# Kernel optimization log

Measured on AMD Instinct MI355X. Metric: run time of the kernel, lower is better.

The kernel has to match this reference:

```python
import jax, jax.numpy as jnp
import numpy as np

B, N, D, H = 64, 1025, 768, 128

def setup_inputs() -> dict:
    key = jax.random.key(0)
    ks = jax.random.split(key, 5)
    x = jax.random.normal(ks[0], (B, N, D), dtype=jnp.float32)
    ln_w = jnp.ones((D,), dtype=jnp.float32)
    ln_b = jnp.zeros((D,), dtype=jnp.float32)
    w1 = jax.random.normal(ks[1], (D, H), dtype=jnp.float32) * (1.0 / np.sqrt(D))
    b1 = jnp.zeros((H,), dtype=jnp.float32)
    w2 = jax.random.normal(ks[2], (H, 1), dtype=jnp.float32) * (1.0 / np.sqrt(H))
    b2 = jnp.zeros((1,), dtype=jnp.float32)
    return {"x": x, "ln_w": ln_w, "ln_b": ln_b, "w1": w1, "b1": b1, "w2": w2, "b2": b2, "k": 256}

def _layernorm(x, w, b, eps=1e-5):
    mu = jnp.mean(x, axis=-1, keepdims=True)
    var = jnp.mean(jnp.square(x - mu), axis=-1, keepdims=True)
    return (x - mu) * jax.lax.rsqrt(var + eps) * w + b

def reference(x, ln_w, ln_b, w1, b1, w2, b2, k):
    Bb, Nn, Dd = x.shape
    h = _layernorm(x, ln_w, ln_b)                      # [B,N,D]
    h = jax.nn.gelu(h @ w1 + b1, approximate=False)    # [B,N,H] (torch GELU = exact erf)
    scores = (h @ w2 + b2).squeeze(-1)                 # [B,N]
    scores = scores.at[:, 0].set(1e9)                  # force CLS kept
    kk = min(k, Nn - 1)
    patch_scores = scores[:, 1:]                       # [B,N-1]
    _, topk_idx = jax.lax.top_k(patch_scores, kk)      # [B,k]
    topk_idx = topk_idx + 1
    cls_idx = jnp.zeros((Bb, 1), dtype=topk_idx.dtype)
    idx_full = jnp.concatenate([cls_idx, topk_idx], axis=1)  # [B,1+k]
    x_reduced = jnp.take_along_axis(x, idx_full[:, :, None], axis=1)  # [B,1+k,D]
    return (x_reduced, idx_full, scores)
```

## Files before the change

kernel.cpp:

```cpp
#include <hip/hip_runtime.h>
#include <hip/hip_bf16.h>
#include <math.h>

#define BB 64
#define NN 1025
#define DD 768
#define HH 128
#define KK 256
#define TOK (BB*NN)
#define OUT_XRED 0
#define OUT_IDX  (BB*(KK+1)*DD)
#define OUT_SC   (OUT_IDX + BB*(KK+1))

typedef float    f32x4 __attribute__((ext_vector_type(4)));
typedef __fp16   h16x2 __attribute__((ext_vector_type(2)));
typedef _Float16 f16x8 __attribute__((ext_vector_type(8)));
#define NSTEP (DD/32)

union U4F { uint4 u; f16x8 h; };
union H2U { h16x2 h; unsigned int u; };

__global__ __launch_bounds__(256) void k_cvtw(const float* __restrict__ w1,
                                              const float* __restrict__ lnw,
                                              unsigned short* __restrict__ wt)
{
    int i = blockIdx.x*256 + threadIdx.x;
    int k = i >> 7, n = i & 127;
    union { _Float16 h; unsigned short s; } c;
    c.h = (_Float16)(w1[i] * lnw[k]);
    int s = k >> 5, g = (k >> 3) & 3, j = k & 7;
    wt[((s*4 + g)*HH + n)*8 + j] = c.s;
}

__global__ __launch_bounds__(1024) void k_cvec(const float* __restrict__ w1,
                                               const float* __restrict__ lnw,
                                               const float* __restrict__ lnb,
                                               const float* __restrict__ b1,
                                               float* __restrict__ cvec)
{
    __shared__ float red[2][8][128];
    const int n = threadIdx.x & 127;
    const int r = threadIdx.x >> 7;
    float s1 = 0.f, s2 = 0.f;
    #pragma unroll 8
    for (int j = 0; j < 96; ++j) {
        int k = r + j*8;
        float wv = w1[k*HH + n];
        s1 = fmaf(lnb[k], wv, s1);
        s2 = fmaf(lnw[k], wv, s2);
    }
    red[0][r][n] = s1;
    red[1][r][n] = s2;
    __syncthreads();
    if (r == 0) {
        float t1 = 0.f, t2 = 0.f;
        #pragma unroll
        for (int q = 0; q < 8; ++q) { t1 += red[0][q][n]; t2 += red[1][q][n]; }
        cvec[n]     = t1 + b1[n];
        cvec[128+n] = t2;
    }
}

__global__ __launch_bounds__(256) void k_fused(const float* __restrict__ x,
    const unsigned short* __restrict__ wt,
    const float* __restrict__ cvec,
    const float* __restrict__ w2, const float* __restrict__ b2,
    float* __restrict__ scores_out)
{
    __shared__ uint4 planes[16*96];
    __shared__ float mus[16], rss[16];
    __shared__ float part[4][16];

    const int tid  = threadIdx.x;
    const int wave = tid >> 6, lane = tid & 63;
    const int g    = lane >> 4, t16 = lane & 15;
    const int t7   = t16 & 7;
    const int tok0 = blockIdx.x * 16;
    const int colbase = wave * 32;
    const int row = tid >> 4, l16 = tid & 15;

    const float4* srow4 = reinterpret_cast<const float4*>(x + (size_t)(tok0 + row) * DD);
    const int rsz = row & 7;
    float s_ = 0.f, ss = 0.f;
    #pragma unroll
    for (int j = 0; j < 6; ++j) {
        float4 a = srow4[l16*2 + j*32];
        float4 b = srow4[l16*2 + j*32 + 1];
        s_ += ((a.x + a.y) + (a.z + a.w)) + ((b.x + b.y) + (b.z + b.w));
        ss += a.x*a.x + a.y*a.y + a.z*a.z + a.w*a.w
            + b.x*b.x + b.y*b.y + b.z*b.z + b.w*b.w;
        H2U h01, h23, h45, h67;
        h01.h = __builtin_amdgcn_cvt_pkrtz(a.x, a.y);
        h23.h = __builtin_amdgcn_cvt_pkrtz(a.z, a.w);
        h45.h = __builtin_amdgcn_cvt_pkrtz(b.x, b.y);
        h67.h = __builtin_amdgcn_cvt_pkrtz(b.z, b.w);
        planes[row*96 + ((l16 + j*16) ^ rsz)] = make_uint4(h01.u, h23.u, h45.u, h67.u);
    }
    #pragma unroll
    for (int m = 8; m; m >>= 1) { s_ += __shfl_xor(s_, m, 64); ss += __shfl_xor(ss, m, 64); }
    const float mu = s_ * (1.0f/768.0f);
    const float rs = 1.0f / sqrtf(ss * (1.0f/768.0f) - mu*mu + 1e-5f);
    if (l16 == 0) { mus[row] = mu; rss[row] = rs; }

    const unsigned short* wtp = wt + ((size_t)g*HH + colbase + t16)*8;
    f16x8 nB0 = *reinterpret_cast<const f16x8*>(wtp);
    f16x8 nB1 = *reinterpret_cast<const f16x8*>(wtp + 128);

    asm volatile("s_waitcnt lgkmcnt(0)" ::: "memory");
    __builtin_amdgcn_s_barrier();

    f32x4 acc0 = {0,0,0,0}, acc1 = {0,0,0,0};
    #pragma unroll
    for (int s = 0; s < NSTEP; ++s) {
        f16x8 B0 = nB0, B1 = nB1;
        if (s + 1 < NSTEP) {
            nB0 = *reinterpret_cast<const f16x8*>(wtp + (size_t)(s+1)*4096);
            nB1 = *reinterpret_cast<const f16x8*>(wtp + (size_t)(s+1)*4096 + 128);
        }
        U4F Ah;
        Ah.u = planes[((s*4 + g) ^ t7) + t16*96];
        acc0 = __builtin_amdgcn_mfma_f32_16x16x32_f16(Ah.h, B0, acc0, 0, 0, 0);
        acc1 = __builtin_amdgcn_mfma_f32_16x16x32_f16(Ah.h, B1, acc1, 0, 0, 0);
    }

    const int c0 = colbase + t16, c1i = colbase + 16 + t16;
    const float c1A = cvec[c0],      c2A = cvec[128 + c0];
    const float c1B = cvec[c1i],     c2B = cvec[128 + c1i];
    const float w2A = w2[c0],        w2B = w2[c1i];
    const float is2 = 0.70710678f;

    float psum[4];
    #pragma unroll
    for (int r = 0; r < 4; ++r) {
        const float mur = mus[g*4 + r], rsr = rss[g*4 + r];
        float v0 = rsr*acc0[r] + c1A - mur*rsr*c2A;
        float v1 = rsr*acc1[r] + c1B - mur*rsr*c2B;
        float g0 = 0.5f * v0 * (1.0f + erff(v0 * is2));
        float g1 = 0.5f * v1 * (1.0f + erff(v1 * is2));
        float p = g0 * w2A + g1 * w2B;
        #pragma unroll
        for (int m = 8; m; m >>= 1) p += __shfl_xor(p, m, 64);
        psum[r] = p;
    }
    if (t16 == 0) {
        #pragma unroll
        for (int r = 0; r < 4; ++r) part[wave][g*4 + r] = psum[r];
    }
    __syncthreads();
    if (tid < 16) {
        float s = part[0][tid] + part[1][tid] + part[2][tid] + part[3][tid] + b2[0];
        int tok = tok0 + tid;
        scores_out[tok] = ((tok % NN) == 0) ? 1.0e9f : s;
    }
}

__global__ __launch_bounds__(1024) void k_topk(const float* __restrict__ scores,
                                               float* __restrict__ idx_out)
{
    __shared__ float sk_[1024];
    __shared__ int   si[1024];
    const int tid = threadIdx.x;
    const int b   = blockIdx.x;
    sk_[tid] = scores[b*NN + 1 + tid];
    si[tid] = tid + 1;
    __syncthreads();
    for (int k = 2; k <= 1024; k <<= 1) {
        for (int j = k >> 1; j > 0; j >>= 1) {
            int ixj = tid ^ j;
            if (ixj > tid) {
                float sa = sk_[tid]; int ia = si[tid];
                float sb = sk_[ixj]; int ib = si[ixj];
                bool beforeB = (sb > sa) || (sb == sa && ib < ia);
                bool dirAsc  = ((tid & k) == 0);
                if (beforeB == dirAsc) {
                    sk_[tid] = sb; si[tid] = ib;
                    sk_[ixj] = sa; si[ixj] = ia;
                }
            }
            __syncthreads();
        }
    }
    if (tid == 0)  idx_out[b*(KK+1)] = 0.0f;
    if (tid < KK)  idx_out[b*(KK+1) + 1 + tid] = (float)si[tid];
}

__global__ __launch_bounds__(192) void k_gather(const float* __restrict__ x,
                                                const float* __restrict__ idx_out,
                                                float* __restrict__ xred)
{
    const int r = blockIdx.x;
    const int b = r / (KK+1);
    const int idx = (int)(idx_out[r] + 0.5f);
    const float4* src = reinterpret_cast<const float4*>(x + ((size_t)b*NN + idx) * DD);
    float4* dst = reinterpret_cast<float4*>(xred + (size_t)r * DD);
    dst[threadIdx.x] = src[threadIdx.x];
}

extern "C" void kernel_launch(void* const* d_in, const int* in_sizes, int n_in,
                              void* d_out, int out_size, void* d_ws, size_t ws_size,
                              hipStream_t stream)
{
    const float* x   = (const float*)d_in[0];
    const float* lnw = (const float*)d_in[1];
    const float* lnb = (const float*)d_in[2];
    const float* w1  = (const float*)d_in[3];
    const float* b1  = (const float*)d_in[4];
    const float* w2  = (const float*)d_in[5];
    const float* b2  = (const float*)d_in[6];

    float* out   = (float*)d_out;
    float* xred  = out + OUT_XRED;
    float* idxf  = out + OUT_IDX;
    float* scout = out + OUT_SC;

    unsigned short* wt = (unsigned short*)d_ws;
    float* cvec = (float*)((char*)d_ws + 196608);

    k_cvtw <<<DD*HH/256, 256, 0, stream>>>(w1, lnw, wt);
    k_cvec <<<1, 1024, 0, stream>>>(w1, lnw, lnb, b1, cvec);
    k_fused<<<TOK/16, 256, 0, stream>>>(x, wt, cvec, w2, b2, scout);
    k_topk <<<BB, 1024, 0, stream>>>(scout, idxf);
    k_gather<<<BB*(KK+1), 192, 0, stream>>>(x, idxf, xred);
}
```

Measured before the change: 95.34 us.

## Merge weight prep kernels and process 32 tokens per fused block

The weight conversion and cvec reduction kernels become one launch: the extra block runs the cvec reduction with only 2 row groups, so its serial loop grows from 96 to 384 steps. The fused LayerNorm+MLP kernel now uses 512 threads covering 32 tokens, with two half-blocks sharing each loaded weight column tile. This saves one launch and halves the block count, but the cvec block now has a longer serial tail and each block uses more LDS.

```diff
diff --git a/kernel.cpp b/kernel.cpp
--- a/kernel.cpp
+++ b/kernel.cpp
@@ -20,64 +20,60 @@
 union U4F { uint4 u; f16x8 h; };
 union H2U { h16x2 h; unsigned int u; };
 
-__global__ __launch_bounds__(256) void k_cvtw(const float* __restrict__ w1,
+__global__ __launch_bounds__(256) void k_prep(const float* __restrict__ w1,
                                               const float* __restrict__ lnw,
-                                              unsigned short* __restrict__ wt)
-{
-    int i = blockIdx.x*256 + threadIdx.x;
-    int k = i >> 7, n = i & 127;
-    union { _Float16 h; unsigned short s; } c;
-    c.h = (_Float16)(w1[i] * lnw[k]);
-    int s = k >> 5, g = (k >> 3) & 3, j = k & 7;
-    wt[((s*4 + g)*HH + n)*8 + j] = c.s;
-}
-
-__global__ __launch_bounds__(1024) void k_cvec(const float* __restrict__ w1,
-                                               const float* __restrict__ lnw,
-                                               const float* __restrict__ lnb,
-                                               const float* __restrict__ b1,
-                                               float* __restrict__ cvec)
-{
-    __shared__ float red[2][8][128];
-    const int n = threadIdx.x & 127;
-    const int r = threadIdx.x >> 7;
-    float s1 = 0.f, s2 = 0.f;
-    #pragma unroll 8
-    for (int j = 0; j < 96; ++j) {
-        int k = r + j*8;
-        float wv = w1[k*HH + n];
-        s1 = fmaf(lnb[k], wv, s1);
-        s2 = fmaf(lnw[k], wv, s2);
-    }
-    red[0][r][n] = s1;
-    red[1][r][n] = s2;
-    __syncthreads();
-    if (r == 0) {
-        float t1 = 0.f, t2 = 0.f;
-        #pragma unroll
-        for (int q = 0; q < 8; ++q) { t1 += red[0][q][n]; t2 += red[1][q][n]; }
-        cvec[n]     = t1 + b1[n];
-        cvec[128+n] = t2;
-    }
-}
-
-__global__ __launch_bounds__(256) void k_fused(const float* __restrict__ x,
+                                              const float* __restrict__ lnb,
+                                              const float* __restrict__ b1,
+                                              unsigned short* __restrict__ wt,
+                                              float* __restrict__ cvec)
+{
+    if (blockIdx.x < 384) {
+        int i = blockIdx.x*256 + threadIdx.x;
+        int k = i >> 7, n = i & 127;
+        union { _Float16 h; unsigned short s; } c;
+        c.h = (_Float16)(w1[i] * lnw[k]);
+        int s = k >> 5, g = (k >> 3) & 3, j = k & 7;
+        wt[((s*4 + g)*HH + n)*8 + j] = c.s;
+    } else {
+        __shared__ float red[2][2][128];
+        const int n = threadIdx.x & 127;
+        const int r = threadIdx.x >> 7;
+        float s1 = 0.f, s2 = 0.f;
+        #pragma unroll 8
+        for (int j = 0; j < 384; ++j) {
+            int k = r + j*2;
+            float wv = w1[k*HH + n];
+            s1 = fmaf(lnb[k], wv, s1);
+            s2 = fmaf(lnw[k], wv, s2);
+        }
+        red[0][r][n] = s1;
+        red[1][r][n] = s2;
+        __syncthreads();
+        if (r == 0) {
+            cvec[n]     = red[0][0][n] + red[0][1][n] + b1[n];
+            cvec[128+n] = red[1][0][n] + red[1][1][n];
+        }
+    }
+}
+
+__global__ __launch_bounds__(512) void k_fused(const float* __restrict__ x,
     const unsigned short* __restrict__ wt,
     const float* __restrict__ cvec,
     const float* __restrict__ w2, const float* __restrict__ b2,
     float* __restrict__ scores_out)
 {
-    __shared__ uint4 planes[16*96];
-    __shared__ float mus[16], rss[16];
-    __shared__ float part[4][16];
+    __shared__ uint4 planes[32*96];
+    __shared__ float mus[32], rss[32];
+    __shared__ float part[8][16];
 
     const int tid  = threadIdx.x;
     const int wave = tid >> 6, lane = tid & 63;
     const int g    = lane >> 4, t16 = lane & 15;
     const int t7   = t16 & 7;
-    const int tok0 = blockIdx.x * 16;
-    const int colbase = wave * 32;
-    const int row = tid >> 4, l16 = tid & 15;
+    const int tok0 = blockIdx.x * 32;
+    const int h    = wave >> 2;
+    const int colbase = (wave & 3) * 32;
+    const int row  = tid >> 4, l16 = tid & 15;
 
     const float4* srow4 = reinterpret_cast<const float4*>(x + (size_t)(tok0 + row) * DD);
     const int rsz = row & 7;
@@ -109,6 +105,7 @@
     asm volatile("s_waitcnt lgkmcnt(0)" ::: "memory");
     __builtin_amdgcn_s_barrier();
 
+    const int arow = (h*16 + t16) * 96;
     f32x4 acc0 = {0,0,0,0}, acc1 = {0,0,0,0};
     #pragma unroll
     for (int s = 0; s < NSTEP; ++s) {
@@ -118,7 +115,7 @@
             nB1 = *reinterpret_cast<const f16x8*>(wtp + (size_t)(s+1)*4096 + 128);
         }
         U4F Ah;
-        Ah.u = planes[((s*4 + g) ^ t7) + t16*96];
+        Ah.u = planes[arow + ((s*4 + g) ^ t7)];
         acc0 = __builtin_amdgcn_mfma_f32_16x16x32_f16(Ah.h, B0, acc0, 0, 0, 0);
         acc1 = __builtin_amdgcn_mfma_f32_16x16x32_f16(Ah.h, B1, acc1, 0, 0, 0);
     }
@@ -132,7 +129,8 @@
     float psum[4];
     #pragma unroll
     for (int r = 0; r < 4; ++r) {
-        const float mur = mus[g*4 + r], rsr = rss[g*4 + r];
+        const int trow = h*16 + g*4 + r;
+        const float mur = mus[trow], rsr = rss[trow];
         float v0 = rsr*acc0[r] + c1A - mur*rsr*c2A;
         float v1 = rsr*acc1[r] + c1B - mur*rsr*c2B;
         float g0 = 0.5f * v0 * (1.0f + erff(v0 * is2));
@@ -147,8 +145,10 @@
         for (int r = 0; r < 4; ++r) part[wave][g*4 + r] = psum[r];
     }
     __syncthreads();
-    if (tid < 16) {
-        float s = part[0][tid] + part[1][tid] + part[2][tid] + part[3][tid] + b2[0];
+    if (tid < 32) {
+        const int hh = tid >> 4, i16 = tid & 15;
+        float s = part[hh*4+0][i16] + part[hh*4+1][i16]
+                + part[hh*4+2][i16] + part[hh*4+3][i16] + b2[0];
         int tok = tok0 + tid;
         scores_out[tok] = ((tok % NN) == 0) ? 1.0e9f : s;
     }
@@ -216,9 +216,8 @@
     unsigned short* wt = (unsigned short*)d_ws;
     float* cvec = (float*)((char*)d_ws + 196608);
 
-    k_cvtw <<<DD*HH/256, 256, 0, stream>>>(w1, lnw, wt);
-    k_cvec <<<1, 1024, 0, stream>>>(w1, lnw, lnb, b1, cvec);
-    k_fused<<<TOK/16, 256, 0, stream>>>(x, wt, cvec, w2, b2, scout);
+    k_prep <<<385, 256, 0, stream>>>(w1, lnw, lnb, b1, wt, cvec);
+    k_fused<<<TOK/32, 512, 0, stream>>>(x, wt, cvec, w2, b2, scout);
     k_topk <<<BB, 1024, 0, stream>>>(scout, idxf);
     k_gather<<<BB*(KK+1), 192, 0, stream>>>(x, idxf, xred);
 }
```

New measurement: 101.6 us. +6.6%, slower.

## Make fused scorer loop over token tiles and prefetch next tile's x

Applied to the files above, without the earlier changes.

The fused layernorm/MLP scoring kernel now launches 1024 blocks instead of one per 16-token tile. Each block processes four tiles, and the first four blocks take one extra tile to cover all 4100. While the MFMA and GELU epilogue run on the current tile, the x rows for the next tile are loaded into registers, so global loads overlap with compute. Per-block constants (cvec, w2, b2) are also loaded once per block instead of once per tile. The cost is 48 extra live float registers per thread, which may lower occupancy, and the four blocks with an extra tile create a small tail.

```diff
diff --git a/kernel.cpp b/kernel.cpp
--- a/kernel.cpp
+++ b/kernel.cpp
@@ -75,82 +75,114 @@
     const int wave = tid >> 6, lane = tid & 63;
     const int g    = lane >> 4, t16 = lane & 15;
     const int t7   = t16 & 7;
-    const int tok0 = blockIdx.x * 16;
     const int colbase = wave * 32;
     const int row = tid >> 4, l16 = tid & 15;
-
-    const float4* srow4 = reinterpret_cast<const float4*>(x + (size_t)(tok0 + row) * DD);
     const int rsz = row & 7;
-    float s_ = 0.f, ss = 0.f;
-    #pragma unroll
-    for (int j = 0; j < 6; ++j) {
-        float4 a = srow4[l16*2 + j*32];
-        float4 b = srow4[l16*2 + j*32 + 1];
-        s_ += ((a.x + a.y) + (a.z + a.w)) + ((b.x + b.y) + (b.z + b.w));
-        ss += a.x*a.x + a.y*a.y + a.z*a.z + a.w*a.w
-            + b.x*b.x + b.y*b.y + b.z*b.z + b.w*b.w;
-        H2U h01, h23, h45, h67;
-        h01.h = __builtin_amdgcn_cvt_pkrtz(a.x, a.y);
-        h23.h = __builtin_amdgcn_cvt_pkrtz(a.z, a.w);
-        h45.h = __builtin_amdgcn_cvt_pkrtz(b.x, b.y);
-        h67.h = __builtin_amdgcn_cvt_pkrtz(b.z, b.w);
-        planes[row*96 + ((l16 + j*16) ^ rsz)] = make_uint4(h01.u, h23.u, h45.u, h67.u);
-    }
-    #pragma unroll
-    for (int m = 8; m; m >>= 1) { s_ += __shfl_xor(s_, m, 64); ss += __shfl_xor(ss, m, 64); }
-    const float mu = s_ * (1.0f/768.0f);
-    const float rs = 1.0f / sqrtf(ss * (1.0f/768.0f) - mu*mu + 1e-5f);
-    if (l16 == 0) { mus[row] = mu; rss[row] = rs; }
-
+    const int bid = blockIdx.x;
+
+    const int c0 = colbase + t16, c1i = colbase + 16 + t16;
+    const float c1A = cvec[c0],  c2A = cvec[128 + c0];
+    const float c1B = cvec[c1i], c2B = cvec[128 + c1i];
+    const float w2A = w2[c0],    w2B = w2[c1i];
+    const float b2v = b2[0];
+    const float is2 = 0.70710678f;
     const unsigned short* wtp = wt + ((size_t)g*HH + colbase + t16)*8;
-    f16x8 nB0 = *reinterpret_cast<const f16x8*>(wtp);
-    f16x8 nB1 = *reinterpret_cast<const f16x8*>(wtp + 128);
-
-    asm volatile("s_waitcnt lgkmcnt(0)" ::: "memory");
-    __builtin_amdgcn_s_barrier();
-
-    f32x4 acc0 = {0,0,0,0}, acc1 = {0,0,0,0};
-    #pragma unroll
-    for (int s = 0; s < NSTEP; ++s) {
-        f16x8 B0 = nB0, B1 = nB1;
-        if (s + 1 < NSTEP) {
-            nB0 = *reinterpret_cast<const f16x8*>(wtp + (size_t)(s+1)*4096);
-            nB1 = *reinterpret_cast<const f16x8*>(wtp + (size_t)(s+1)*4096 + 128);
-        }
-        U4F Ah;
-        Ah.u = planes[((s*4 + g) ^ t7) + t16*96];
-        acc0 = __builtin_amdgcn_mfma_f32_16x16x32_f16(Ah.h, B0, acc0, 0, 0, 0);
-        acc1 = __builtin_amdgcn_mfma_f32_16x16x32_f16(Ah.h, B1, acc1, 0, 0, 0);
-    }
-
-    const int c0 = colbase + t16, c1i = colbase + 16 + t16;
-    const float c1A = cvec[c0],      c2A = cvec[128 + c0];
-    const float c1B = cvec[c1i],     c2B = cvec[128 + c1i];
-    const float w2A = w2[c0],        w2B = w2[c1i];
-    const float is2 = 0.70710678f;
-
-    float psum[4];
-    #pragma unroll
-    for (int r = 0; r < 4; ++r) {
-        const float mur = mus[g*4 + r], rsr = rss[g*4 + r];
-        float v0 = rsr*acc0[r] + c1A - mur*rsr*c2A;
-        float v1 = rsr*acc1[r] + c1B - mur*rsr*c2B;
-        float g0 = 0.5f * v0 * (1.0f + erff(v0 * is2));
-        float g1 = 0.5f * v1 * (1.0f + erff(v1 * is2));
-        float p = g0 * w2A + g1 * w2B;
-        #pragma unroll
-        for (int m = 8; m; m >>= 1) p += __shfl_xor(p, m, 64);
-        psum[r] = p;
-    }
-    if (t16 == 0) {
-        #pragma unroll
-        for (int r = 0; r < 4; ++r) part[wave][g*4 + r] = psum[r];
-    }
-    __syncthreads();
-    if (tid < 16) {
-        float s = part[0][tid] + part[1][tid] + part[2][tid] + part[3][tid] + b2[0];
-        int tok = tok0 + tid;
-        scores_out[tok] = ((tok % NN) == 0) ? 1.0e9f : s;
+
+    const int nt = 4 + (bid < 4);
+
+    {
+        const float4* srow4 = reinterpret_cast<const float4*>(
+            x + ((size_t)(bid*4)*16 + row) * DD);
+    }
+    float4 xa[6], xb[6];
+    {
+        const float4* srow4 = reinterpret_cast<const float4*>(
+            x + ((size_t)(bid*4)*16 + row) * DD);
+        #pragma unroll
+        for (int j = 0; j < 6; ++j) {
+            xa[j] = srow4[l16*2 + j*32];
+            xb[j] = srow4[l16*2 + j*32 + 1];
+        }
+    }
+
+    for (int t = 0; t < nt; ++t) {
+        const int tile = (t < 4) ? (bid*4 + t) : (4096 + bid);
+        const int tok0 = tile * 16;
+
+        float s_ = 0.f, ss = 0.f;
+        #pragma unroll
+        for (int j = 0; j < 6; ++j) {
+            float4 a = xa[j], b = xb[j];
+            s_ += ((a.x + a.y) + (a.z + a.w)) + ((b.x + b.y) + (b.z + b.w));
+            ss += a.x*a.x + a.y*a.y + a.z*a.z + a.w*a.w
+                + b.x*b.x + b.y*b.y + b.z*b.z + b.w*b.w;
+            H2U h01, h23, h45, h67;
+            h01.h = __builtin_amdgcn_cvt_pkrtz(a.x, a.y);
+            h23.h = __builtin_amdgcn_cvt_pkrtz(a.z, a.w);
+            h45.h = __builtin_amdgcn_cvt_pkrtz(b.x, b.y);
+            h67.h = __builtin_amdgcn_cvt_pkrtz(b.z, b.w);
+            planes[row*96 + ((l16 + j*16) ^ rsz)] = make_uint4(h01.u, h23.u, h45.u, h67.u);
+        }
+        #pragma unroll
+        for (int m = 8; m; m >>= 1) { s_ += __shfl_xor(s_, m, 64); ss += __shfl_xor(ss, m, 64); }
+        const float mu = s_ * (1.0f/768.0f);
+        const float rs = 1.0f / sqrtf(ss * (1.0f/768.0f) - mu*mu + 1e-5f);
+        if (l16 == 0) { mus[row] = mu; rss[row] = rs; }
+
+        asm volatile("s_waitcnt lgkmcnt(0)" ::: "memory");
+        __builtin_amdgcn_s_barrier();
+
+        f32x4 acc0 = {0,0,0,0}, acc1 = {0,0,0,0};
+        f16x8 nB0 = *reinterpret_cast<const f16x8*>(wtp);
+        f16x8 nB1 = *reinterpret_cast<const f16x8*>(wtp + 128);
+        #pragma unroll
+        for (int s = 0; s < NSTEP; ++s) {
+            f16x8 B0 = nB0, B1 = nB1;
+            if (s + 1 < NSTEP) {
+                nB0 = *reinterpret_cast<const f16x8*>(wtp + (size_t)(s+1)*4096);
+                nB1 = *reinterpret_cast<const f16x8*>(wtp + (size_t)(s+1)*4096 + 128);
+            }
+            U4F Ah;
+            Ah.u = planes[((s*4 + g) ^ t7) + t16*96];
+            acc0 = __builtin_amdgcn_mfma_f32_16x16x32_f16(Ah.h, B0, acc0, 0, 0, 0);
+            acc1 = __builtin_amdgcn_mfma_f32_16x16x32_f16(Ah.h, B1, acc1, 0, 0, 0);
+        }
+
+        __builtin_amdgcn_sched_barrier(0);
+        if (t + 1 < nt) {
+            const int ntile = (t + 1 < 4) ? (bid*4 + t + 1) : (4096 + bid);
+            const float4* nrow4 = reinterpret_cast<const float4*>(
+                x + ((size_t)ntile*16 + row) * DD);
+            #pragma unroll
+            for (int j = 0; j < 6; ++j) {
+                xa[j] = nrow4[l16*2 + j*32];
+                xb[j] = nrow4[l16*2 + j*32 + 1];
+            }
+        }
+
+        float psum[4];
+        #pragma unroll
+        for (int r = 0; r < 4; ++r) {
+            const float mur = mus[g*4 + r], rsr = rss[g*4 + r];
+            float v0 = rsr*acc0[r] + c1A - mur*rsr*c2A;
+            float v1 = rsr*acc1[r] + c1B - mur*rsr*c2B;
+            float g0 = 0.5f * v0 * (1.0f + erff(v0 * is2));
+            float g1 = 0.5f * v1 * (1.0f + erff(v1 * is2));
+            float p = g0 * w2A + g1 * w2B;
+            #pragma unroll
+            for (int m = 8; m; m >>= 1) p += __shfl_xor(p, m, 64);
+            psum[r] = p;
+        }
+        if (t16 == 0) {
+            #pragma unroll
+            for (int r = 0; r < 4; ++r) part[wave][g*4 + r] = psum[r];
+        }
+        __syncthreads();
+        if (tid < 16) {
+            float sv = part[0][tid] + part[1][tid] + part[2][tid] + part[3][tid] + b2v;
+            int tok = tok0 + tid;
+            scores_out[tok] = ((tok % NN) == 0) ? 1.0e9f : sv;
+        }
     }
 }
 
@@ -218,7 +250,7 @@
 
     k_cvtw <<<DD*HH/256, 256, 0, stream>>>(w1, lnw, wt);
     k_cvec <<<1, 1024, 0, stream>>>(w1, lnw, lnb, b1, cvec);
-    k_fused<<<TOK/16, 256, 0, stream>>>(x, wt, cvec, w2, b2, scout);
+    k_fused<<<1024, 256, 0, stream>>>(x, wt, cvec, w2, b2, scout);
     k_topk <<<BB, 1024, 0, stream>>>(scout, idxf);
     k_gather<<<BB*(KK+1), 192, 0, stream>>>(x, idxf, xred);
 }
```

After: 103.5 us. 8.6% more time.

## Split fused LN+MLP scoring into fp16 pack kernel and MFMA scoring kernel

Applied to the files above, without the earlier changes.

Splits the fused kernel into two. k_pack reads x, computes per-token mean and rstd, and writes an fp16 copy of x to workspace, already laid out in MFMA operand order. k_score streams those operands straight from global memory with register prefetch and no LDS round trip, then applies the LN correction, GELU and the w2 dot product. This drops the LDS staging and barrier from the MFMA loop, but adds an extra global write and read of about 100MB of fp16 data plus one more launch.

```diff
diff --git a/kernel.cpp b/kernel.cpp
--- a/kernel.cpp
+++ b/kernel.cpp
@@ -61,26 +61,17 @@
     }
 }
 
-__global__ __launch_bounds__(256) void k_fused(const float* __restrict__ x,
-    const unsigned short* __restrict__ wt,
-    const float* __restrict__ cvec,
-    const float* __restrict__ w2, const float* __restrict__ b2,
-    float* __restrict__ scores_out)
+__global__ __launch_bounds__(256) void k_pack(const float* __restrict__ x,
+                                              float2* __restrict__ mr,
+                                              uint4* __restrict__ xh)
 {
     __shared__ uint4 planes[16*96];
-    __shared__ float mus[16], rss[16];
-    __shared__ float part[4][16];
-
-    const int tid  = threadIdx.x;
-    const int wave = tid >> 6, lane = tid & 63;
-    const int g    = lane >> 4, t16 = lane & 15;
-    const int t7   = t16 & 7;
+    const int tid = threadIdx.x;
+    const int row = tid >> 4, l16 = tid & 15;
+    const int rsz = row & 7;
     const int tok0 = blockIdx.x * 16;
-    const int colbase = wave * 32;
-    const int row = tid >> 4, l16 = tid & 15;
 
     const float4* srow4 = reinterpret_cast<const float4*>(x + (size_t)(tok0 + row) * DD);
-    const int rsz = row & 7;
     float s_ = 0.f, ss = 0.f;
     #pragma unroll
     for (int j = 0; j < 6; ++j) {
@@ -100,39 +91,64 @@
     for (int m = 8; m; m >>= 1) { s_ += __shfl_xor(s_, m, 64); ss += __shfl_xor(ss, m, 64); }
     const float mu = s_ * (1.0f/768.0f);
     const float rs = 1.0f / sqrtf(ss * (1.0f/768.0f) - mu*mu + 1e-5f);
-    if (l16 == 0) { mus[row] = mu; rss[row] = rs; }
-
+    if (l16 == 0) mr[tok0 + row] = make_float2(mu, rs);
+    __syncthreads();
+
+    const int cw = tid >> 4, t16p = tid & 15, sz2 = t16p & 7;
+    uint4* dst = xh + (size_t)blockIdx.x * 1536;
+    #pragma unroll
+    for (int jj = 0; jj < 6; ++jj) {
+        const int c = cw + jj*16;
+        dst[c*16 + t16p] = planes[t16p*96 + (c ^ sz2)];
+    }
+}
+
+__global__ __launch_bounds__(256) void k_score(const uint4* __restrict__ xh,
+    const unsigned short* __restrict__ wt,
+    const float* __restrict__ cvec,
+    const float* __restrict__ w2, const float* __restrict__ b2,
+    const float2* __restrict__ mr,
+    float* __restrict__ scores_out)
+{
+    const int tid  = threadIdx.x;
+    const int wave = tid >> 6, lane = tid & 63;
+    const int g    = lane >> 4, t16 = lane & 15;
+    const int tok0 = blockIdx.x * 16;
+    const int colbase = wave * 32;
+
+    const uint4* ap = xh + (size_t)blockIdx.x * 1536 + g*16 + t16;
     const unsigned short* wtp = wt + ((size_t)g*HH + colbase + t16)*8;
+
+    f32x4 acc0 = {0,0,0,0}, acc1 = {0,0,0,0};
+    U4F nA; nA.u = ap[0];
     f16x8 nB0 = *reinterpret_cast<const f16x8*>(wtp);
     f16x8 nB1 = *reinterpret_cast<const f16x8*>(wtp + 128);
 
-    asm volatile("s_waitcnt lgkmcnt(0)" ::: "memory");
-    __builtin_amdgcn_s_barrier();
-
-    f32x4 acc0 = {0,0,0,0}, acc1 = {0,0,0,0};
     #pragma unroll
     for (int s = 0; s < NSTEP; ++s) {
+        U4F A = nA;
         f16x8 B0 = nB0, B1 = nB1;
         if (s + 1 < NSTEP) {
+            nA.u = ap[(s+1)*64];
             nB0 = *reinterpret_cast<const f16x8*>(wtp + (size_t)(s+1)*4096);
             nB1 = *reinterpret_cast<const f16x8*>(wtp + (size_t)(s+1)*4096 + 128);
         }
-        U4F Ah;
-        Ah.u = planes[((s*4 + g) ^ t7) + t16*96];
-        acc0 = __builtin_amdgcn_mfma_f32_16x16x32_f16(Ah.h, B0, acc0, 0, 0, 0);
-        acc1 = __builtin_amdgcn_mfma_f32_16x16x32_f16(Ah.h, B1, acc1, 0, 0, 0);
+        acc0 = __builtin_amdgcn_mfma_f32_16x16x32_f16(A.h, B0, acc0, 0, 0, 0);
+        acc1 = __builtin_amdgcn_mfma_f32_16x16x32_f16(A.h, B1, acc1, 0, 0, 0);
     }
 
     const int c0 = colbase + t16, c1i = colbase + 16 + t16;
-    const float c1A = cvec[c0],      c2A = cvec[128 + c0];
-    const float c1B = cvec[c1i],     c2B = cvec[128 + c1i];
-    const float w2A = w2[c0],        w2B = w2[c1i];
+    const float c1A = cvec[c0],  c2A = cvec[128 + c0];
+    const float c1B = cvec[c1i], c2B = cvec[128 + c1i];
+    const float w2A = w2[c0],    w2B = w2[c1i];
     const float is2 = 0.70710678f;
 
+    __shared__ float part[4][16];
     float psum[4];
     #pragma unroll
     for (int r = 0; r < 4; ++r) {
-        const float mur = mus[g*4 + r], rsr = rss[g*4 + r];
+        const float2 m2 = mr[tok0 + g*4 + r];
+        const float mur = m2.x, rsr = m2.y;
         float v0 = rsr*acc0[r] + c1A - mur*rsr*c2A;
         float v1 = rsr*acc1[r] + c1B - mur*rsr*c2B;
         float g0 = 0.5f * v0 * (1.0f + erff(v0 * is2));
@@ -213,12 +229,16 @@
     float* idxf  = out + OUT_IDX;
     float* scout = out + OUT_SC;
 
-    unsigned short* wt = (unsigned short*)d_ws;
-    float* cvec = (float*)((char*)d_ws + 196608);
+    char* wsb = (char*)d_ws;
+    unsigned short* wt = (unsigned short*)wsb;
+    float* cvec = (float*)(wsb + 196608);
+    float2* mr  = (float2*)(wsb + 197632);
+    uint4* xh   = (uint4*)(wsb + 722432);
 
     k_cvtw <<<DD*HH/256, 256, 0, stream>>>(w1, lnw, wt);
     k_cvec <<<1, 1024, 0, stream>>>(w1, lnw, lnb, b1, cvec);
-    k_fused<<<TOK/16, 256, 0, stream>>>(x, wt, cvec, w2, b2, scout);
+    k_pack <<<TOK/16, 256, 0, stream>>>(x, mr, xh);
+    k_score<<<TOK/16, 256, 0, stream>>>(xh, wt, cvec, w2, b2, mr, scout);
     k_topk <<<BB, 1024, 0, stream>>>(scout, idxf);
     k_gather<<<BB*(KK+1), 192, 0, stream>>>(x, idxf, xred);
 }
```

New measurement: 143.2 us. 50.2% more time.
